# Optimization experiments

Measured on AMD Instinct MI355X. Metric: run time of the kernel, lower is better.

## Reference

```python
import jax, jax.numpy as jnp
import numpy as np

N_NODES = 100000
N_GRAPHS = 1000
NPG = 100           # nodes per graph (fixed)
N_EDGES = 3200000   # avg degree 32
F_IN = 128
K = 30              # SortAggregation k
N_CLASSES = 10


def setup_inputs() -> dict:
    key = jax.random.key(0)
    ks = jax.random.split(key, 24)
    x = jax.random.normal(ks[0], (N_NODES, F_IN), jnp.float32)
    # edges constrained within each 100-node graph
    g = jax.random.randint(ks[1], (N_EDGES,), 0, N_GRAPHS)
    src = g * NPG + jax.random.randint(ks[2], (N_EDGES,), 0, NPG)
    dst = g * NPG + jax.random.randint(ks[3], (N_EDGES,), 0, NPG)
    edge_index = jnp.stack([src, dst]).astype(jnp.int32)
    batch = jnp.repeat(jnp.arange(N_GRAPHS, dtype=jnp.int32), NPG)

    def lin(k, fi, fo):
        return jax.random.normal(k, (fi, fo), jnp.float32) / np.sqrt(fi)

    return {
        "x": x, "edge_index": edge_index, "batch": batch,
        "W1": lin(ks[4], F_IN, 32), "b1": jnp.zeros((32,), jnp.float32),
        "W2": lin(ks[5], 32, 32),   "b2": jnp.zeros((32,), jnp.float32),
        "W3": lin(ks[6], 32, 32),   "b3": jnp.zeros((32,), jnp.float32),
        "W4": lin(ks[7], 32, 1),    "b4": jnp.zeros((1,), jnp.float32),
        "conv5_w": jax.random.normal(ks[8], (16, 1, 97), jnp.float32) / np.sqrt(97.0),
        "conv5_b": jnp.zeros((16,), jnp.float32),
        "conv6_w": jax.random.normal(ks[9], (32, 16, 5), jnp.float32) / np.sqrt(16 * 5.0),
        "conv6_b": jnp.zeros((32,), jnp.float32),
        "fc1_w": lin(ks[10], 352, 128), "fc1_b": jnp.zeros((128,), jnp.float32),
        "fc2_w": lin(ks[11], 128, N_CLASSES), "fc2_b": jnp.zeros((N_CLASSES,), jnp.float32),
    }


def reference(x, edge_index, batch,
              W1, b1, W2, b2, W3, b3, W4, b4,
              conv5_w, conv5_b, conv6_w, conv6_b,
              fc1_w, fc1_b, fc2_w, fc2_b):
    N = x.shape[0]
    src, dst = edge_index[0], edge_index[1]
    # remove_self_loops -> zero edge weight; GCNConv then re-adds self loops (weight 1)
    w = jnp.where(src == dst, 0.0, 1.0).astype(x.dtype)
    deg = jax.ops.segment_sum(w, dst, num_segments=N) + 1.0  # includes self loop
    dis = jax.lax.rsqrt(deg)
    norm = w * dis[src] * dis[dst]        # per-edge D^-1/2 A D^-1/2
    self_norm = dis * dis                 # self-loop coefficient 1/deg

    def gcn(h, W, b):
        h = h @ W                                   # [N, out]
        agg = jax.ops.segment_sum(norm[:, None] * h[src], dst, num_segments=N)
        return agg + self_norm[:, None] * h + b

    x1 = jnp.tanh(gcn(x, W1, b1))
    x2 = jnp.tanh(gcn(x1, W2, b2))
    x3 = jnp.tanh(gcn(x2, W3, b3))
    x4 = jnp.tanh(gcn(x3, W4, b4))
    h = jnp.concatenate([x1, x2, x3, x4], axis=-1)  # [N, 97]
    C = h.shape[-1]

    # SortAggregation(k=30): per graph, sort nodes by last channel descending, keep top k
    xs = h.reshape(N_GRAPHS, NPG, C)
    order = jnp.argsort(-xs[..., -1], axis=1)[:, :K]            # [B, K]
    pooled = jnp.take_along_axis(xs, order[:, :, None], axis=1)  # [B, K, C]
    y = pooled.reshape(N_GRAPHS, 1, K * C)                       # [B, 1, 2910]

    dn = ('NCH', 'OIH', 'NCH')
    y = jax.lax.conv_general_dilated(y, conv5_w, (97,), 'VALID', dimension_numbers=dn)
    y = jax.nn.relu(y + conv5_b[None, :, None])                  # [B, 16, 30]
    B, Co, L = y.shape
    y = y.reshape(B, Co, L // 2, 2).max(axis=-1)                 # maxpool(2,2) -> [B,16,15]
    y = jax.lax.conv_general_dilated(y, conv6_w, (1,), 'VALID', dimension_numbers=dn)
    y = jax.nn.relu(y + conv6_b[None, :, None])                  # [B, 32, 11]
    y = y.reshape(B, -1)                                         # [B, 352]
    out = jax.nn.relu(y @ fc1_w + fc1_b)                         # dropout = identity (eval)
    return jax.nn.log_softmax(out @ fc2_w + fc2_b, axis=-1)
```

## Files before the change

### kernel.cpp

```cpp
#include <hip/hip_runtime.h>

#define N_GRAPHS_C 1000
#define NPG_C      100
#define N_EDGES_C  3200000
#define KTOP_C     30
#define CAP        4096

typedef _Float16 f16x8 __attribute__((ext_vector_type(8)));
typedef float    f32x4 __attribute__((ext_vector_type(4)));
typedef _Float16 h2_t  __attribute__((ext_vector_type(2)));

__device__ __forceinline__ float fdot2u(unsigned a, unsigned b, float c) {
#if __has_builtin(__builtin_amdgcn_fdot2)
    return __builtin_amdgcn_fdot2(__builtin_bit_cast(h2_t, a),
                                  __builtin_bit_cast(h2_t, b), c, false);
#else
    h2_t ha = __builtin_bit_cast(h2_t, a), hb = __builtin_bit_cast(h2_t, b);
    return fmaf((float)ha.x, (float)hb.x, fmaf((float)ha.y, (float)hb.y, c));
#endif
}

__device__ __forceinline__ unsigned packh2(float x, float y) {
    _Float16 hx = (_Float16)x, hy = (_Float16)y;
    return (unsigned)__builtin_bit_cast(unsigned short, hx) |
           ((unsigned)__builtin_bit_cast(unsigned short, hy) << 16);
}

__device__ __forceinline__ float f16b(unsigned v) {
    return (float)__builtin_bit_cast(_Float16, (unsigned short)v);
}

__device__ __forceinline__ float ftanh(float x) {
    float e = __expf(2.0f * x);
    return 1.0f - 2.0f * __builtin_amdgcn_rcpf(e + 1.0f);
}

__device__ __forceinline__ void split8(const float* v, f16x8& h, f16x8& l) {
    #pragma unroll
    for (int j = 0; j < 8; ++j) {
        _Float16 hh = (_Float16)v[j];
        h[j] = hh;
        l[j] = (_Float16)(v[j] - (float)hh);
    }
}


__global__ __launch_bounds__(1024)
void bucket_kernel(const int* __restrict__ src, const int* __restrict__ dst,
                   int* __restrict__ gcur, unsigned short* __restrict__ slots) {
    __shared__ int hist[N_GRAPHS_C];
    const int tid = threadIdx.x;
    const int base = blockIdx.x * 8192;
    for (int i = tid; i < N_GRAPHS_C; i += 1024) hist[i] = 0;
    __syncthreads();

    int g[8]; unsigned short pk[8]; bool v[8];
    #pragma unroll
    for (int k = 0; k < 8; ++k) {
        int e = base + tid + k * 1024;
        v[k] = false;
        if (e < N_EDGES_C) {
            int s = src[e], d = dst[e];
            if (s != d) {
                int gg = s / NPG_C;
                g[k] = gg;
                pk[k] = (unsigned short)(((d - gg * NPG_C) << 7) | (s - gg * NPG_C));
                v[k] = true;
                atomicAdd(&hist[gg], 1);
            }
        }
    }
    __syncthreads();
    for (int i = tid; i < N_GRAPHS_C; i += 1024) {
        int c = hist[i];
        hist[i] = atomicAdd(&gcur[i], c);
    }
    __syncthreads();
    #pragma unroll
    for (int k = 0; k < 8; ++k) {
        if (v[k]) {
            int pos = atomicAdd(&hist[g[k]], 1);
            if (pos < CAP) slots[g[k] * CAP + pos] = pk[k];
        }
    }
}

#define SMEM_WORDS 16112

extern "C" __global__ __launch_bounds__(512, 4)
void dgcnn_kernel(const float* __restrict__ x,
                  const int* __restrict__ gcur, const unsigned short* __restrict__ slots,
                  const float* __restrict__ W1, const float* __restrict__ b1,
                  const float* __restrict__ W2, const float* __restrict__ b2,
                  const float* __restrict__ W3, const float* __restrict__ b3,
                  const float* __restrict__ W4, const float* __restrict__ b4,
                  const float* __restrict__ w5, const float* __restrict__ b5,
                  const float* __restrict__ w6, const float* __restrict__ b6,
                  const float* __restrict__ fw1, const float* __restrict__ fb1,
                  const float* __restrict__ fw2, const float* __restrict__ fb2,
                  float* __restrict__ out)
{
    extern __shared__ unsigned smu[];
    unsigned* cntP   = smu;
    unsigned* planes = smu + 7616;
    float* xrows  = (float*)(smu + 11968);
    float* pooled = (float*)(smu + 11968);
    float* dis = (float*)(smu + 15568);
    float* t4  = (float*)(smu + 15680);
    unsigned* t4h = smu + 15784;
    unsigned* t4l = smu + 15848;
    float* sX4 = (float*)(smu + 15912);
    int*   srank = (int*)(smu + 16012);
    float* s5  = (float*)smu;
    float* sPb = s5 + 480;
    float* s6  = s5 + 720;
    float* sO1 = s5 + 1072;
    float* sFc = s5 + 1200;
    float* sZ  = s5 + 1712;

    const int tid = threadIdx.x;
    const int g   = blockIdx.x;
    const int l64 = tid & 63;
    const int wv  = tid >> 6;

    const float* xg = x + (size_t)g * NPG_C * 128;

    for (int idx = tid; idx < 11968; idx += 512) smu[idx] = 0u;
    if (tid < 12) dis[100 + tid] = 0.f;
    __syncthreads();

    {
        int ec = gcur[g]; if (ec > CAP) ec = CAP;
        for (int k = tid; k < ec; k += 512) {
            unsigned e = slots[g * CAP + k];
            unsigned idx = (e >> 7) * 104 + (e & 127);
            atomicAdd(&planes[idx >> 2], 1u << ((idx & 3) * 8));
        }
    }
    __syncthreads();

    if (tid < 100) {
        const unsigned* rw = planes + tid * 26;
        unsigned s = 0;
        #pragma unroll
        for (int k = 0; k < 26; ++k) {
            unsigned v = rw[k];
            s += (v & 0xffu) + ((v >> 8) & 0xffu) + ((v >> 16) & 0xffu) + (v >> 24);
        }
        dis[tid] = rsqrtf((float)s + 1.0f);
    }
    __syncthreads();

    #pragma unroll
    for (int k = 0; k < 6; ++k) {
        int w = tid + k * 512;
        if (w < 2600) {
            unsigned v = planes[w];
            int i = w / 26, c = w - i * 26;
            int d = i * 68 + c * 2;
            cntP[d]     = packh2((float)(v & 255u), (float)((v >> 8) & 255u));
            cntP[d + 1] = packh2((float)((v >> 16) & 255u), (float)(v >> 24));
        }
    }
    __syncthreads();

    auto packStore = [&](f32x4 c, int n, int r0, float4 dv) {
        float v0 = c[0]*dv.x, v1 = c[1]*dv.y, v2 = c[2]*dv.z, v3 = c[3]*dv.w;
        _Float16 h0=(_Float16)v0, h1=(_Float16)v1, h2=(_Float16)v2, h3=(_Float16)v3;
        uint2 wh, wl;
        wh.x = (unsigned)__builtin_bit_cast(unsigned short,h0) |
               ((unsigned)__builtin_bit_cast(unsigned short,h1) << 16);
        wh.y = (unsigned)__builtin_bit_cast(unsigned short,h2) |
               ((unsigned)__builtin_bit_cast(unsigned short,h3) << 16);
        wl.x = packh2(v0-(float)h0, v1-(float)h1);
        wl.y = packh2(v2-(float)h2, v3-(float)h3);
        *(uint2*)&planes[n*68 + (r0>>1)] = wh;
        *(uint2*)&planes[2176 + n*68 + (r0>>1)] = wl;
    };

    for (int idx = tid; idx < 768; idx += 512) {
        int rw = idx / 12, wd = idx - rw * 12;
        planes[rw * 68 + 56 + wd] = 0u;
    }
    if (wv < 7) {
        f32x4 c0 = {0.f,0.f,0.f,0.f}, c1 = {0.f,0.f,0.f,0.f};
        const int arow = (wv << 4) + (l64 & 15);
        const int kq   = (l64 >> 4) << 3;
        const int bn   = l64 & 15;
        const bool aok = arow < 100;
        #pragma unroll
        for (int kc = 0; kc < 4; ++kc) {
            const int kb = (kc << 5) + kq;
            float av[8];
            if (aok) {
                float4 xa = *(const float4*)&xg[arow*128 + kb];
                float4 xb = *(const float4*)&xg[arow*128 + kb + 4];
                av[0]=xa.x; av[1]=xa.y; av[2]=xa.z; av[3]=xa.w;
                av[4]=xb.x; av[5]=xb.y; av[6]=xb.z; av[7]=xb.w;
            } else {
                #pragma unroll
                for (int j = 0; j < 8; ++j) av[j] = 0.f;
            }
            f16x8 ah, al; split8(av, ah, al);
            float b0[8], b1[8];
            #pragma unroll
            for (int i = 0; i < 8; ++i) {
                b0[i] = W1[(kb+i)*32 + bn];
                b1[i] = W1[(kb+i)*32 + 16 + bn];
            }
            f16x8 b0h,b0l,b1h,b1l; split8(b0,b0h,b0l); split8(b1,b1h,b1l);
            c0 = __builtin_amdgcn_mfma_f32_16x16x32_f16(ah, b0h, c0, 0, 0, 0);
            c0 = __builtin_amdgcn_mfma_f32_16x16x32_f16(al, b0h, c0, 0, 0, 0);
            c0 = __builtin_amdgcn_mfma_f32_16x16x32_f16(ah, b0l, c0, 0, 0, 0);
            c1 = __builtin_amdgcn_mfma_f32_16x16x32_f16(ah, b1h, c1, 0, 0, 0);
            c1 = __builtin_amdgcn_mfma_f32_16x16x32_f16(al, b1h, c1, 0, 0, 0);
            c1 = __builtin_amdgcn_mfma_f32_16x16x32_f16(ah, b1l, c1, 0, 0, 0);
        }
        const int r0 = (wv << 4) + ((l64 >> 4) << 2);
        float4 dv = *(const float4*)&dis[r0];
        packStore(c0, bn,      r0, dv);
        packStore(c1, bn + 16, r0, dv);
    }
    __syncthreads();

    auto AGG = [&](f32x4& fa, f32x4& fb, const float* Bp, bool wx) {
        if (wv < 7) {
            f32x4 a0 = {0.f,0.f,0.f,0.f}, a1 = {0.f,0.f,0.f,0.f};
            const unsigned* ab = cntP + ((wv << 4) + (l64 & 15)) * 68 + ((l64 >> 4) << 2);
            const unsigned* bb = planes + (l64 & 15) * 68 + ((l64 >> 4) << 2);
            #pragma unroll
            for (int p = 0; p < 2; ++p) {
                const unsigned* bp = bb + p * 2176;
                #pragma unroll
                for (int ks = 0; ks < 4; ++ks) {
                    f16x8 av = __builtin_bit_cast(f16x8, *(const uint4*)(ab + ks*16));
                    f16x8 b0 = __builtin_bit_cast(f16x8, *(const uint4*)(bp + ks*16));
                    f16x8 b1 = __builtin_bit_cast(f16x8, *(const uint4*)(bp + 16*68 + ks*16));
                    a0 = __builtin_amdgcn_mfma_f32_16x16x32_f16(av, b0, a0, 0, 0, 0);
                    a1 = __builtin_amdgcn_mfma_f32_16x16x32_f16(av, b1, a1, 0, 0, 0);
                }
            }
            int n0 = l64 & 15, r0 = (wv << 4) + ((l64 >> 4) << 2);
            uint2 sh0 = *(const uint2*)(planes + n0 * 68 + (r0 >> 1));
            uint2 sl0 = *(const uint2*)(planes + 2176 + n0 * 68 + (r0 >> 1));
            uint2 sh1 = *(const uint2*)(planes + (16 + n0) * 68 + (r0 >> 1));
            uint2 sl1 = *(const uint2*)(planes + 2176 + (16 + n0) * 68 + (r0 >> 1));
            float4 dv = *(const float4*)&dis[r0];
            float bi0 = Bp[n0], bi1 = Bp[16 + n0];
            #pragma unroll
            for (int j = 0; j < 4; ++j) {
                unsigned sft = (unsigned)((j & 1) * 16);
                float sc0 = f16b(((j < 2) ? sh0.x : sh0.y) >> sft) +
                            f16b(((j < 2) ? sl0.x : sl0.y) >> sft);
                float sc1 = f16b(((j < 2) ? sh1.x : sh1.y) >> sft) +
                            f16b(((j < 2) ? sl1.x : sl1.y) >> sft);
                float d_ = (j == 0) ? dv.x : (j == 1) ? dv.y : (j == 2) ? dv.z : dv.w;
                float v0 = ftanh(d_ * (a0[j] + sc0) + bi0);
                float v1 = ftanh(d_ * (a1[j] + sc1) + bi1);
                fa[j] = v0; fb[j] = v1;
                if (wx) {
                    int row = r0 + j;
                    if (row < 100) { xrows[row*36 + n0] = v0; xrows[row*36 + 16 + n0] = v1; }
                }
            }
        }
    };

    auto XWm = [&](const float* W) {
        if (wv < 7) {
            f32x4 c0 = {0.f,0.f,0.f,0.f}, c1 = {0.f,0.f,0.f,0.f};
            const int arow = (wv << 4) + (l64 & 15);
            const int kq   = (l64 >> 4) << 3;
            const int bn   = l64 & 15;
            float av[8];
            if (arow < 100) {
                float4 xa = *(const float4*)&xrows[arow*36 + kq];
                float4 xb = *(const float4*)&xrows[arow*36 + kq + 4];
                av[0]=xa.x; av[1]=xa.y; av[2]=xa.z; av[3]=xa.w;
                av[4]=xb.x; av[5]=xb.y; av[6]=xb.z; av[7]=xb.w;
            } else {
                #pragma unroll
                for (int j = 0; j < 8; ++j) av[j] = 0.f;
            }
            f16x8 ah, al; split8(av, ah, al);
            float b0[8], b1[8];
            #pragma unroll
            for (int i = 0; i < 8; ++i) {
                b0[i] = W[(kq+i)*32 + bn];
                b1[i] = W[(kq+i)*32 + 16 + bn];
            }
            f16x8 b0h,b0l,b1h,b1l; split8(b0,b0h,b0l); split8(b1,b1h,b1l);
            c0 = __builtin_amdgcn_mfma_f32_16x16x32_f16(ah, b0h, c0, 0, 0, 0);
            c0 = __builtin_amdgcn_mfma_f32_16x16x32_f16(al, b0h, c0, 0, 0, 0);
            c0 = __builtin_amdgcn_mfma_f32_16x16x32_f16(ah, b0l, c0, 0, 0, 0);
            c1 = __builtin_amdgcn_mfma_f32_16x16x32_f16(ah, b1h, c1, 0, 0, 0);
            c1 = __builtin_amdgcn_mfma_f32_16x16x32_f16(al, b1h, c1, 0, 0, 0);
            c1 = __builtin_amdgcn_mfma_f32_16x16x32_f16(ah, b1l, c1, 0, 0, 0);
            const int r0 = (wv << 4) + ((l64 >> 4) << 2);
            float4 dv = *(const float4*)&dis[r0];
            packStore(c0, bn,      r0, dv);
            packStore(c1, bn + 16, r0, dv);
        }
    };

    f32x4 f1a, f1b, f2a, f2b, f3a, f3b;

    AGG(f1a, f1b, b1, true);   __syncthreads();
    XWm(W2);                   __syncthreads();
    AGG(f2a, f2b, b2, true);   __syncthreads();
    XWm(W3);                   __syncthreads();
    AGG(f3a, f3b, b3, false);

    if (wv < 7) {
        float w4a = W4[l64 & 15], w4b = W4[16 + (l64 & 15)];
        int r0 = (wv << 4) + ((l64 >> 4) << 2);
        #pragma unroll
        for (int j = 0; j < 4; ++j) {
            float v = f3a[j] * w4a + f3b[j] * w4b;
            v += __shfl_xor(v, 1, 16); v += __shfl_xor(v, 2, 16);
            v += __shfl_xor(v, 4, 16); v += __shfl_xor(v, 8, 16);
            int row = r0 + j;
            if ((l64 & 15) == 0 && row < 100) t4[row] = v * dis[row];
        }
    }
    if (tid < 100) srank[tid] = 0;
    __syncthreads();

    if (tid < 64) {
        float a = (2*tid < 100) ? t4[2*tid] : 0.f;
        float b = (2*tid+1 < 100) ? t4[2*tid+1] : 0.f;
        _Float16 ah = (_Float16)a, bh = (_Float16)b;
        t4h[tid] = (unsigned)__builtin_bit_cast(unsigned short, ah) |
                   ((unsigned)__builtin_bit_cast(unsigned short, bh) << 16);
        t4l[tid] = packh2(a - (float)ah, b - (float)bh);
    }
    __syncthreads();

    if (tid < 100) {
        float acc = 0.f;
        const unsigned* cr = cntP + tid * 68;
        for (int kc = 0; kc < 16; ++kc) {
            uint4 cw = *(const uint4*)&cr[kc*4];
            uint4 th = *(const uint4*)&t4h[kc*4];
            uint4 tl = *(const uint4*)&t4l[kc*4];
            acc = fdot2u(cw.x, th.x, acc);
            acc = fdot2u(cw.y, th.y, acc);
            acc = fdot2u(cw.z, th.z, acc);
            acc = fdot2u(cw.w, th.w, acc);
            acc = fdot2u(cw.x, tl.x, acc);
            acc = fdot2u(cw.y, tl.y, acc);
            acc = fdot2u(cw.z, tl.z, acc);
            acc = fdot2u(cw.w, tl.w, acc);
        }
        sX4[tid] = tanhf(dis[tid] * (acc + t4[tid]) + b4[0]);
    }
    __syncthreads();

    if (tid < 500) {
        int i = tid / 5, seg = tid - i * 5;
        float vi = sX4[i];
        int c = 0, jb = seg * 20;
        #pragma unroll
        for (int jo = 0; jo < 20; ++jo) {
            int j = jb + jo;
            float vj = sX4[j];
            c += (vj > vi) || (vj == vi && j < i);
        }
        atomicAdd(&srank[i], c);
    }
    __syncthreads();

    if (wv < 7) {
        int n0 = l64 & 15, r0 = (wv << 4) + ((l64 >> 4) << 2);
        #pragma unroll
        for (int j = 0; j < 4; ++j) {
            int row = r0 + j;
            if (row < 100) {
                int rk = srank[row];
                if (rk < KTOP_C) {
                    float* pr = pooled + rk * 100;
                    pr[n0]      = f1a[j]; pr[16 + n0] = f1b[j];
                    pr[32 + n0] = f2a[j]; pr[48 + n0] = f2b[j];
                    pr[64 + n0] = f3a[j]; pr[80 + n0] = f3b[j];
                    if (n0 == 0) pr[96] = sX4[row];
                }
            }
        }
    }
    __syncthreads();

    if (tid < 480) {
        int l = tid >> 4, co = tid & 15;
        const float* pr = pooled + l * 100;
        const float* wr = w5 + co * 97;
        float acc = b5[co];
        for (int c4 = 0; c4 < 96; c4 += 4) {
            const float4 pv = *(const float4*)&pr[c4];
            acc = fmaf(pv.x, wr[c4+0], fmaf(pv.y, wr[c4+1], fmaf(pv.z, wr[c4+2], fmaf(pv.w, wr[c4+3], acc))));
        }
        acc = fmaf(pr[96], wr[96], acc);
        s5[co * 30 + l] = fmaxf(acc, 0.f);
    }
    __syncthreads();

    if (tid < 240) {
        int co = tid / 15, j = tid - co * 15;
        sPb[co * 15 + j] = fmaxf(s5[co * 30 + 2*j], s5[co * 30 + 2*j + 1]);
    }
    __syncthreads();

    if (tid < 352) {
        int co = tid / 11, l = tid - co * 11;
        float acc = b6[co];
        for (int ci = 0; ci < 16; ++ci) {
            const float* wr = w6 + (co * 16 + ci) * 5;
            const float* pr = sPb + ci * 15 + l;
            acc = fmaf(wr[0], pr[0], fmaf(wr[1], pr[1], fmaf(wr[2], pr[2],
                  fmaf(wr[3], pr[3], fmaf(wr[4], pr[4], acc)))));
        }
        s6[co * 11 + l] = fmaxf(acc, 0.f);
    }
    __syncthreads();

    {
        int j = tid & 127, part = tid >> 7;
        int ibeg = part * 88, iend = ibeg + 88;
        float acc = (part == 0) ? fb1[j] : 0.f;
        for (int i = ibeg; i < iend; ++i)
            acc = fmaf(s6[i], fw1[i * 128 + j], acc);
        sFc[part * 128 + j] = acc;
    }
    __syncthreads();
    if (tid < 128) {
        float v = sFc[tid] + sFc[128 + tid] + sFc[256 + tid] + sFc[384 + tid];
        sO1[tid] = fmaxf(v, 0.f);
    }
    __syncthreads();

    if (tid < 10) {
        float acc = fb2[tid];
        for (int k = 0; k < 128; ++k)
            acc = fmaf(sO1[k], fw2[k * 10 + tid], acc);
        sZ[tid] = acc;
    }
    __syncthreads();
    if (tid < 10) {
        float m = sZ[0];
        for (int c = 1; c < 10; ++c) m = fmaxf(m, sZ[c]);
        float se = 0.f;
        for (int c = 0; c < 10; ++c) se += expf(sZ[c] - m);
        out[g * 10 + tid] = sZ[tid] - m - logf(se);
    }
}

extern "C" void kernel_launch(void* const* d_in, const int* in_sizes, int n_in,
                              void* d_out, int out_size, void* d_ws, size_t ws_size,
                              hipStream_t stream) {
    const float* x   = (const float*)d_in[0];
    const int*   ei  = (const int*)d_in[1];
    const int*   src = ei;
    const int*   dst = ei + N_EDGES_C;
    const float* W1 = (const float*)d_in[3];  const float* b1 = (const float*)d_in[4];
    const float* W2 = (const float*)d_in[5];  const float* b2 = (const float*)d_in[6];
    const float* W3 = (const float*)d_in[7];  const float* b3 = (const float*)d_in[8];
    const float* W4 = (const float*)d_in[9];  const float* b4 = (const float*)d_in[10];
    const float* w5 = (const float*)d_in[11]; const float* b5 = (const float*)d_in[12];
    const float* w6 = (const float*)d_in[13]; const float* b6 = (const float*)d_in[14];
    const float* fw1 = (const float*)d_in[15]; const float* fb1 = (const float*)d_in[16];
    const float* fw2 = (const float*)d_in[17]; const float* fb2 = (const float*)d_in[18];
    float* out = (float*)d_out;

    int* gcur = (int*)d_ws;
    unsigned short* slots = (unsigned short*)((char*)d_ws + 4096);

    hipMemsetAsync(gcur, 0, 4096, stream);

    bucket_kernel<<<(N_EDGES_C + 8191) / 8192, 1024, 0, stream>>>(src, dst, gcur, slots);

    size_t smem = (size_t)SMEM_WORDS * sizeof(unsigned);
    hipFuncSetAttribute((const void*)dgcnn_kernel,
                        hipFuncAttributeMaxDynamicSharedMemorySize, (int)smem);
    dgcnn_kernel<<<N_GRAPHS_C, 512, smem, stream>>>(
        x, gcur, slots, W1, b1, W2, b2, W3, b3, W4, b4,
        w5, b5, w6, b6, fw1, fb1, fw2, fb2, out);
}
```

Measured before the change: 112.2 us.

## Presplit GCN weights to fp16 hi/lo, MFMA the final aggregation, stage conv weights in LDS

Adds a one-block prep kernel that splits W1/W2/W3 into packed fp16 high and low planes. The main kernel now loads those with vector loads instead of doing strided scalar loads and splitting them in every block. The fourth-layer aggregation moves from a per-thread fdot2 loop to MFMA, and the degree reduction is spread over 400 threads using atomics. Conv5, conv6 and fc2 weights are copied into shared memory before the readout. The trade-off is an extra kernel launch and some LDS reuse, and the MFMA path does wasted work on zero-filled B columns.

```diff
diff --git a/kernel.cpp b/kernel.cpp
--- a/kernel.cpp
+++ b/kernel.cpp
@@ -8,17 +8,6 @@
 
 typedef _Float16 f16x8 __attribute__((ext_vector_type(8)));
 typedef float    f32x4 __attribute__((ext_vector_type(4)));
-typedef _Float16 h2_t  __attribute__((ext_vector_type(2)));
-
-__device__ __forceinline__ float fdot2u(unsigned a, unsigned b, float c) {
-#if __has_builtin(__builtin_amdgcn_fdot2)
-    return __builtin_amdgcn_fdot2(__builtin_bit_cast(h2_t, a),
-                                  __builtin_bit_cast(h2_t, b), c, false);
-#else
-    h2_t ha = __builtin_bit_cast(h2_t, a), hb = __builtin_bit_cast(h2_t, b);
-    return fmaf((float)ha.x, (float)hb.x, fmaf((float)ha.y, (float)hb.y, c));
-#endif
-}
 
 __device__ __forceinline__ unsigned packh2(float x, float y) {
     _Float16 hx = (_Float16)x, hy = (_Float16)y;
@@ -85,14 +74,44 @@
     }
 }
 
+__global__ __launch_bounds__(512)
+void wprep_kernel(const float* __restrict__ W1, const float* __restrict__ W2,
+                  const float* __restrict__ W3, unsigned* __restrict__ wp) {
+    const int t = threadIdx.x;
+    for (int w = t; w < 2048; w += 512) {
+        int n = w >> 6, kp = w & 63, k = kp * 2;
+        float a = W1[k*32 + n], b = W1[(k+1)*32 + n];
+        _Float16 ah = (_Float16)a, bh = (_Float16)b;
+        wp[w]        = (unsigned)__builtin_bit_cast(unsigned short, ah) |
+                       ((unsigned)__builtin_bit_cast(unsigned short, bh) << 16);
+        wp[2048 + w] = packh2(a - (float)ah, b - (float)bh);
+    }
+    for (int w = t; w < 512; w += 512) {
+        int n = w >> 4, kp = w & 15, k = kp * 2;
+        float a = W2[k*32 + n], b = W2[(k+1)*32 + n];
+        _Float16 ah = (_Float16)a, bh = (_Float16)b;
+        wp[4096 + w] = (unsigned)__builtin_bit_cast(unsigned short, ah) |
+                       ((unsigned)__builtin_bit_cast(unsigned short, bh) << 16);
+        wp[4608 + w] = packh2(a - (float)ah, b - (float)bh);
+    }
+    for (int w = t; w < 512; w += 512) {
+        int n = w >> 4, kp = w & 15, k = kp * 2;
+        float a = W3[k*32 + n], b = W3[(k+1)*32 + n];
+        _Float16 ah = (_Float16)a, bh = (_Float16)b;
+        wp[5120 + w] = (unsigned)__builtin_bit_cast(unsigned short, ah) |
+                       ((unsigned)__builtin_bit_cast(unsigned short, bh) << 16);
+        wp[5632 + w] = packh2(a - (float)ah, b - (float)bh);
+    }
+}
+
 #define SMEM_WORDS 16112
 
 extern "C" __global__ __launch_bounds__(512, 4)
 void dgcnn_kernel(const float* __restrict__ x,
                   const int* __restrict__ gcur, const unsigned short* __restrict__ slots,
-                  const float* __restrict__ W1, const float* __restrict__ b1,
-                  const float* __restrict__ W2, const float* __restrict__ b2,
-                  const float* __restrict__ W3, const float* __restrict__ b3,
+                  const unsigned* __restrict__ wp,
+                  const float* __restrict__ b1, const float* __restrict__ b2,
+                  const float* __restrict__ b3,
                   const float* __restrict__ W4, const float* __restrict__ b4,
                   const float* __restrict__ w5, const float* __restrict__ b5,
                   const float* __restrict__ w6, const float* __restrict__ b6,
@@ -117,6 +136,12 @@
     float* sO1 = s5 + 1072;
     float* sFc = s5 + 1200;
     float* sZ  = s5 + 1712;
+    float* w5s = (float*)(smu + 1728);
+    float* b5s = (float*)(smu + 3280);
+    float* w6s = (float*)(smu + 3296);
+    float* b6s = (float*)(smu + 5856);
+    float* fw2s = (float*)(smu + 7616);
+    float* fb2s = (float*)(smu + 8896);
 
     const int tid = threadIdx.x;
     const int g   = blockIdx.x;
@@ -124,9 +149,12 @@
     const int wv  = tid >> 6;
 
     const float* xg = x + (size_t)g * NPG_C * 128;
+    const unsigned* w1h = wp;
+    const unsigned* w1l = wp + 2048;
 
     for (int idx = tid; idx < 11968; idx += 512) smu[idx] = 0u;
     if (tid < 12) dis[100 + tid] = 0.f;
+    if (tid < 100) srank[tid] = 0;
     __syncthreads();
 
     {
@@ -139,15 +167,16 @@
     }
     __syncthreads();
 
-    if (tid < 100) {
-        const unsigned* rw = planes + tid * 26;
+    if (tid < 400) {
+        int row = tid >> 2, part = tid & 3;
+        int wb = part * 7, we = (part == 3) ? 26 : wb + 7;
+        const unsigned* rw = planes + row * 26;
         unsigned s = 0;
-        #pragma unroll
-        for (int k = 0; k < 26; ++k) {
+        for (int k = wb; k < we; ++k) {
             unsigned v = rw[k];
             s += (v & 0xffu) + ((v >> 8) & 0xffu) + ((v >> 16) & 0xffu) + (v >> 24);
         }
-        dis[tid] = rsqrtf((float)s + 1.0f);
+        atomicAdd(&srank[row], (int)s);
     }
     __syncthreads();
 
@@ -162,6 +191,7 @@
             cntP[d + 1] = packh2((float)((v >> 16) & 255u), (float)(v >> 24));
         }
     }
+    if (tid < 100) dis[tid] = rsqrtf((float)srank[tid] + 1.0f);
     __syncthreads();
 
     auto packStore = [&](f32x4 c, int n, int r0, float4 dv) {
@@ -191,24 +221,22 @@
         #pragma unroll
         for (int kc = 0; kc < 4; ++kc) {
             const int kb = (kc << 5) + kq;
-            float av[8];
+            f16x8 ah, al;
             if (aok) {
+                float av[8];
                 float4 xa = *(const float4*)&xg[arow*128 + kb];
                 float4 xb = *(const float4*)&xg[arow*128 + kb + 4];
                 av[0]=xa.x; av[1]=xa.y; av[2]=xa.z; av[3]=xa.w;
                 av[4]=xb.x; av[5]=xb.y; av[6]=xb.z; av[7]=xb.w;
+                split8(av, ah, al);
             } else {
                 #pragma unroll
-                for (int j = 0; j < 8; ++j) av[j] = 0.f;
-            }
-            f16x8 ah, al; split8(av, ah, al);
-            float b0[8], b1[8];
-            #pragma unroll
-            for (int i = 0; i < 8; ++i) {
-                b0[i] = W1[(kb+i)*32 + bn];
-                b1[i] = W1[(kb+i)*32 + 16 + bn];
-            }
-            f16x8 b0h,b0l,b1h,b1l; split8(b0,b0h,b0l); split8(b1,b1h,b1l);
+                for (int j = 0; j < 8; ++j) { ah[j] = (_Float16)0.f; al[j] = (_Float16)0.f; }
+            }
+            f16x8 b0h = __builtin_bit_cast(f16x8, *(const uint4*)(w1h + bn*64 + (kb>>1)));
+            f16x8 b0l = __builtin_bit_cast(f16x8, *(const uint4*)(w1l + bn*64 + (kb>>1)));
+            f16x8 b1h = __builtin_bit_cast(f16x8, *(const uint4*)(w1h + (bn+16)*64 + (kb>>1)));
+            f16x8 b1l = __builtin_bit_cast(f16x8, *(const uint4*)(w1l + (bn+16)*64 + (kb>>1)));
             c0 = __builtin_amdgcn_mfma_f32_16x16x32_f16(ah, b0h, c0, 0, 0, 0);
             c0 = __builtin_amdgcn_mfma_f32_16x16x32_f16(al, b0h, c0, 0, 0, 0);
             c0 = __builtin_amdgcn_mfma_f32_16x16x32_f16(ah, b0l, c0, 0, 0, 0);
@@ -266,30 +294,28 @@
         }
     };
 
-    auto XWm = [&](const float* W) {
+    auto XWm = [&](const unsigned* wh, const unsigned* wl) {
         if (wv < 7) {
             f32x4 c0 = {0.f,0.f,0.f,0.f}, c1 = {0.f,0.f,0.f,0.f};
             const int arow = (wv << 4) + (l64 & 15);
             const int kq   = (l64 >> 4) << 3;
             const int bn   = l64 & 15;
-            float av[8];
+            f16x8 ah, al;
             if (arow < 100) {
+                float av[8];
                 float4 xa = *(const float4*)&xrows[arow*36 + kq];
                 float4 xb = *(const float4*)&xrows[arow*36 + kq + 4];
                 av[0]=xa.x; av[1]=xa.y; av[2]=xa.z; av[3]=xa.w;
                 av[4]=xb.x; av[5]=xb.y; av[6]=xb.z; av[7]=xb.w;
+                split8(av, ah, al);
             } else {
                 #pragma unroll
-                for (int j = 0; j < 8; ++j) av[j] = 0.f;
-            }
-            f16x8 ah, al; split8(av, ah, al);
-            float b0[8], b1[8];
-            #pragma unroll
-            for (int i = 0; i < 8; ++i) {
-                b0[i] = W[(kq+i)*32 + bn];
-                b1[i] = W[(kq+i)*32 + 16 + bn];
-            }
-            f16x8 b0h,b0l,b1h,b1l; split8(b0,b0h,b0l); split8(b1,b1h,b1l);
+                for (int j = 0; j < 8; ++j) { ah[j] = (_Float16)0.f; al[j] = (_Float16)0.f; }
+            }
+            f16x8 b0h = __builtin_bit_cast(f16x8, *(const uint4*)(wh + bn*16 + (kq>>1)));
+            f16x8 b0l = __builtin_bit_cast(f16x8, *(const uint4*)(wl + bn*16 + (kq>>1)));
+            f16x8 b1h = __builtin_bit_cast(f16x8, *(const uint4*)(wh + (bn+16)*16 + (kq>>1)));
+            f16x8 b1l = __builtin_bit_cast(f16x8, *(const uint4*)(wl + (bn+16)*16 + (kq>>1)));
             c0 = __builtin_amdgcn_mfma_f32_16x16x32_f16(ah, b0h, c0, 0, 0, 0);
             c0 = __builtin_amdgcn_mfma_f32_16x16x32_f16(al, b0h, c0, 0, 0, 0);
             c0 = __builtin_amdgcn_mfma_f32_16x16x32_f16(ah, b0l, c0, 0, 0, 0);
@@ -305,10 +331,10 @@
 
     f32x4 f1a, f1b, f2a, f2b, f3a, f3b;
 
-    AGG(f1a, f1b, b1, true);   __syncthreads();
-    XWm(W2);                   __syncthreads();
-    AGG(f2a, f2b, b2, true);   __syncthreads();
-    XWm(W3);                   __syncthreads();
+    AGG(f1a, f1b, b1, true);        __syncthreads();
+    XWm(wp + 4096, wp + 4608);      __syncthreads();
+    AGG(f2a, f2b, b2, true);        __syncthreads();
+    XWm(wp + 5120, wp + 5632);      __syncthreads();
     AGG(f3a, f3b, b3, false);
 
     if (wv < 7) {
@@ -323,7 +349,6 @@
             if ((l64 & 15) == 0 && row < 100) t4[row] = v * dis[row];
         }
     }
-    if (tid < 100) srank[tid] = 0;
     __syncthreads();
 
     if (tid < 64) {
@@ -334,25 +359,36 @@
                    ((unsigned)__builtin_bit_cast(unsigned short, bh) << 16);
         t4l[tid] = packh2(a - (float)ah, b - (float)bh);
     }
-    __syncthreads();
-
-    if (tid < 100) {
-        float acc = 0.f;
-        const unsigned* cr = cntP + tid * 68;
-        for (int kc = 0; kc < 16; ++kc) {
-            uint4 cw = *(const uint4*)&cr[kc*4];
-            uint4 th = *(const uint4*)&t4h[kc*4];
-            uint4 tl = *(const uint4*)&t4l[kc*4];
-            acc = fdot2u(cw.x, th.x, acc);
-            acc = fdot2u(cw.y, th.y, acc);
-            acc = fdot2u(cw.z, th.z, acc);
-            acc = fdot2u(cw.w, th.w, acc);
-            acc = fdot2u(cw.x, tl.x, acc);
-            acc = fdot2u(cw.y, tl.y, acc);
-            acc = fdot2u(cw.z, tl.z, acc);
-            acc = fdot2u(cw.w, tl.w, acc);
-        }
-        sX4[tid] = tanhf(dis[tid] * (acc + t4[tid]) + b4[0]);
+    if (tid < 100) srank[tid] = 0;
+    __syncthreads();
+
+    if (wv < 7) {
+        f32x4 c = {0.f,0.f,0.f,0.f};
+        const unsigned* ab = cntP + ((wv << 4) + (l64 & 15)) * 68 + ((l64 >> 4) << 2);
+        const int kq = (l64 >> 4) << 3;
+        const bool bz = (l64 & 15) == 0;
+        #pragma unroll
+        for (int ks = 0; ks < 4; ++ks) {
+            f16x8 av = __builtin_bit_cast(f16x8, *(const uint4*)(ab + ks*16));
+            f16x8 bh, bl;
+            if (bz) {
+                bh = __builtin_bit_cast(f16x8, *(const uint4*)(t4h + ks*16 + (kq>>1)));
+                bl = __builtin_bit_cast(f16x8, *(const uint4*)(t4l + ks*16 + (kq>>1)));
+            } else {
+                #pragma unroll
+                for (int j = 0; j < 8; ++j) { bh[j] = (_Float16)0.f; bl[j] = (_Float16)0.f; }
+            }
+            c = __builtin_amdgcn_mfma_f32_16x16x32_f16(av, bh, c, 0, 0, 0);
+            c = __builtin_amdgcn_mfma_f32_16x16x32_f16(av, bl, c, 0, 0, 0);
+        }
+        if (bz) {
+            int r0 = (wv << 4) + ((l64 >> 4) << 2);
+            #pragma unroll
+            for (int j = 0; j < 4; ++j) {
+                int row = r0 + j;
+                if (row < 100) sX4[row] = tanhf(dis[row] * (c[j] + t4[row]) + b4[0]);
+            }
+        }
     }
     __syncthreads();
 
@@ -368,6 +404,12 @@
         }
         atomicAdd(&srank[i], c);
     }
+    for (int k = tid; k < 1552; k += 512) w5s[k] = w5[k];
+    if (tid < 16)  b5s[tid] = b5[tid];
+    for (int k = tid; k < 2560; k += 512) w6s[k] = w6[k];
+    if (tid < 32)  b6s[tid] = b6[tid];
+    for (int k = tid; k < 1280; k += 512) fw2s[k] = fw2[k];
+    if (tid < 10)  fb2s[tid] = fb2[tid];
     __syncthreads();
 
     if (wv < 7) {
@@ -392,8 +434,8 @@
     if (tid < 480) {
         int l = tid >> 4, co = tid & 15;
         const float* pr = pooled + l * 100;
-        const float* wr = w5 + co * 97;
-        float acc = b5[co];
+        const float* wr = w5s + co * 97;
+        float acc = b5s[co];
         for (int c4 = 0; c4 < 96; c4 += 4) {
             const float4 pv = *(const float4*)&pr[c4];
             acc = fmaf(pv.x, wr[c4+0], fmaf(pv.y, wr[c4+1], fmaf(pv.z, wr[c4+2], fmaf(pv.w, wr[c4+3], acc))));
@@ -411,9 +453,9 @@
 
     if (tid < 352) {
         int co = tid / 11, l = tid - co * 11;
-        float acc = b6[co];
+        float acc = b6s[co];
         for (int ci = 0; ci < 16; ++ci) {
-            const float* wr = w6 + (co * 16 + ci) * 5;
+            const float* wr = w6s + (co * 16 + ci) * 5;
             const float* pr = sPb + ci * 15 + l;
             acc = fmaf(wr[0], pr[0], fmaf(wr[1], pr[1], fmaf(wr[2], pr[2],
                   fmaf(wr[3], pr[3], fmaf(wr[4], pr[4], acc)))));
@@ -438,9 +480,9 @@
     __syncthreads();
 
     if (tid < 10) {
-        float acc = fb2[tid];
+        float acc = fb2s[tid];
         for (int k = 0; k < 128; ++k)
-            acc = fmaf(sO1[k], fw2[k * 10 + tid], acc);
+            acc = fmaf(sO1[k], fw2s[k * 10 + tid], acc);
         sZ[tid] = acc;
     }
     __syncthreads();
@@ -472,15 +514,17 @@
 
     int* gcur = (int*)d_ws;
     unsigned short* slots = (unsigned short*)((char*)d_ws + 4096);
+    unsigned* wpp = (unsigned*)((char*)d_ws + 4096 + (size_t)N_GRAPHS_C * CAP * 2);
 
     hipMemsetAsync(gcur, 0, 4096, stream);
 
     bucket_kernel<<<(N_EDGES_C + 8191) / 8192, 1024, 0, stream>>>(src, dst, gcur, slots);
+    wprep_kernel<<<1, 512, 0, stream>>>(W1, W2, W3, wpp);
 
     size_t smem = (size_t)SMEM_WORDS * sizeof(unsigned);
     hipFuncSetAttribute((const void*)dgcnn_kernel,
                         hipFuncAttributeMaxDynamicSharedMemorySize, (int)smem);
     dgcnn_kernel<<<N_GRAPHS_C, 512, smem, stream>>>(
-        x, gcur, slots, W1, b1, W2, b2, W3, b3, W4, b4,
+        x, gcur, slots, wpp, b1, b2, b3, W4, b4,
         w5, b5, w6, b6, fw1, fb1, fw2, fb2, out);
 }
```

After: 110.1 us. Within noise of the previous version (-1.8%).
